# Kernel tuning notes

Measured on AMD Instinct MI355X. Metric: run time of the kernel, lower is better.

Reference implementation:

```python
import jax, jax.numpy as jnp
import numpy as np

N = 100000   # nodes
E = 1600000  # edges (avg degree 16)
D = 64       # input feature dim
H = 64       # hidden dim


def _uniform(k, shape, fan_in):
    s = 1.0 / np.sqrt(fan_in).astype(np.float32)
    return jax.random.uniform(k, shape, jnp.float32, -s, s)


def setup_inputs() -> dict:
    key = jax.random.key(0)
    ks = jax.random.split(key, 9)
    x = jax.random.normal(ks[0], (N, D), jnp.float32)
    edge_index = jax.random.randint(ks[1], (2, E), 0, N, dtype=jnp.int64)
    edge_weight = jax.random.uniform(ks[2], (E,), jnp.float32)
    return {
        "x": x,
        "edge_index": edge_index,
        "edge_weight": edge_weight,
        # conv1: GraphConv(D, H): lin_rel (with bias) + lin_root (no bias)
        "w1_rel": _uniform(ks[3], (H, D), D),
        "b1": _uniform(ks[4], (H,), D),
        "w1_root": _uniform(ks[5], (H, D), D),
        # conv2: GraphConv(H, H)
        "w2_rel": _uniform(ks[6], (H, H), H),
        "b2": _uniform(ks[7], (H,), H),
        "w2_root": _uniform(ks[8], (H, H), H),
    }


def _graph_conv(h, src, dst, ew, w_rel, b, w_root):
    # PyG GraphConv with aggr='add':
    #   out_i = W_rel @ sum_{(j->i) in E} ew_ji * h_j + b + W_root @ h_i
    msg = h[src] * ew[:, None]                              # [E, F] gather
    agg = jax.ops.segment_sum(msg, dst, num_segments=N)     # [N, F] scatter-add
    return agg @ w_rel.T + b + h @ w_root.T


def reference(x, edge_index, edge_weight, w1_rel, b1, w1_root, w2_rel, b2, w2_root):
    src, dst = edge_index[0], edge_index[1]
    # dropout(0.2) is identity in eval mode
    h = jax.nn.relu(_graph_conv(x, src, dst, edge_weight, w1_rel, b1, w1_root))
    h = jax.nn.relu(_graph_conv(h, src, dst, edge_weight, w2_rel, b2, w2_root))
    return h
```

## Files before the change

kernel.cpp:

```cpp
#include <hip/hip_runtime.h>
#include <cstddef>


#define FDIM 64
#define BSHC 9
#define BNC (1 << BSHC)
#define CAPC 8960

static inline size_t align256(size_t x) { return (x + 255) & ~size_t(255); }

typedef __attribute__((ext_vector_type(8))) short bf16x8;
typedef __attribute__((ext_vector_type(4))) float f32x4;

__device__ __forceinline__ ushort f2bf(float f) {
    unsigned u = __float_as_uint(f);
    unsigned r = u + 0x7fffu + ((u >> 16) & 1u);
    return (ushort)(r >> 16);
}
__device__ __forceinline__ float bflo(unsigned g) { return __uint_as_float(g << 16); }
__device__ __forceinline__ float bfhi(unsigned g) { return __uint_as_float(g & 0xffff0000u); }
__device__ __forceinline__ unsigned packbf(float lo, float hi) {
    return (unsigned)f2bf(lo) | ((unsigned)f2bf(hi) << 16);
}

__global__ void k_detect(const int* __restrict__ ei, int* __restrict__ flag,
                         int* __restrict__ gcur, int nbc) {
    __shared__ int any;
    if (threadIdx.x == 0) any = 0;
    __syncthreads();
    for (int k = threadIdx.x; k < 2048; k += 256) {
        if (ei[2 * k + 1] != 0) any = 1;
    }
    for (int i = threadIdx.x; i < nbc; i += 256) gcur[i] = 0;
    __syncthreads();
    if (threadIdx.x == 0) *flag = (any == 0) ? 1 : 0;
}

__global__ void k_toBf16(const float* __restrict__ in, ushort* __restrict__ outp,
                         int nflt) {
    int i = (blockIdx.x * blockDim.x + threadIdx.x) * 4;
    if (i >= nflt) return;
    float4 v = *reinterpret_cast<const float4*>(in + i);
    ushort4 o;
    o.x = f2bf(v.x); o.y = f2bf(v.y); o.z = f2bf(v.z); o.w = f2bf(v.w);
    *reinterpret_cast<ushort4*>(outp + i) = o;
}

__global__ void k_packW(const float* __restrict__ wrel1, const float* __restrict__ wroot1,
                        const float* __restrict__ wrel2, const float* __restrict__ wroot2,
                        ushort* __restrict__ wp1, ushort* __restrict__ wp2) {
    int tid = blockIdx.x * blockDim.x + threadIdx.x;
    int layer = tid >> 13;
    int idx = tid & 8191;
    int j = idx & 7, l = (idx >> 3) & 63, og = (idx >> 9) & 3, kk = idx >> 11;
    int k = kk * 32 + ((l >> 4) << 3) + j;
    int o = og * 16 + (l & 15);
    const float* rel  = layer ? wrel2 : wrel1;
    const float* root = layer ? wroot2 : wroot1;
    float v = (k < 64) ? rel[o * FDIM + k] : root[o * FDIM + (k - 64)];
    (layer ? wp2 : wp1)[idx] = f2bf(v);
}

__global__ void __launch_bounds__(512)
k_scatterC(const int* __restrict__ ei, const float* __restrict__ ew, int E,
           const int* __restrict__ flag, int* __restrict__ gcur,
           uint2* __restrict__ recs, int nbc) {
    __shared__ int hcnt[256];
    __shared__ int hbase[256];
    int t = threadIdx.x;
    int base = blockIdx.x * 4096;
    int sh = *flag;
    if (t < 256) hcnt[t] = 0;
    __syncthreads();

    int bkt[8];
    uint2 rec[8];
#pragma unroll
    for (int j = 0; j < 8; ++j) {
        int e = base + j * 512 + t;
        bkt[j] = -1;
        if (e < E) {
            int s = ei[(size_t)e << sh];
            int d = ei[(size_t)(E + e) << sh];
            bkt[j] = d >> BSHC;
            rec[j].x = (unsigned)s | ((unsigned)(d & (BNC - 1)) << 17);
            rec[j].y = __float_as_uint(ew[e]);
            atomicAdd(&hcnt[bkt[j]], 1);
        }
    }
    __syncthreads();
    if (t < nbc) {
        int c = hcnt[t];
        hbase[t] = c ? (t * CAPC + atomicAdd(&gcur[t], c)) : 0;
    }
    __syncthreads();
    if (t < 256) hcnt[t] = 0;
    __syncthreads();
#pragma unroll
    for (int j = 0; j < 8; ++j) {
        if (bkt[j] >= 0) {
            int r = atomicAdd(&hcnt[bkt[j]], 1);
            int pos = hbase[bkt[j]] + r;
            if (pos < (bkt[j] + 1) * CAPC) recs[pos] = rec[j];
        }
    }
}

__global__ void __launch_bounds__(512)
k_csrSortC(const int* __restrict__ gcur, uint2* __restrict__ recs, int n,
           int* __restrict__ rs, int* __restrict__ re) {
    __shared__ uint2 lrec[CAPC];
    __shared__ int lh[BNC];
    __shared__ int lo[BNC];
    __shared__ int lcur[BNC];
    int b = blockIdx.x, t = threadIdx.x;
    int base = b * CAPC;
    int cnt = gcur[b];
    if (cnt > CAPC) cnt = CAPC;

    for (int i = t; i < cnt; i += 512) lrec[i] = recs[base + i];
    lh[t] = 0;
    __syncthreads();
    for (int i = t; i < cnt; i += 512) atomicAdd(&lh[lrec[i].x >> 17], 1);
    __syncthreads();
    lo[t] = lh[t];
    __syncthreads();
    for (int off = 1; off < BNC; off <<= 1) {
        int v = (t >= off) ? lo[t - off] : 0;
        __syncthreads();
        lo[t] += v;
        __syncthreads();
    }
    {
        int ex = lo[t] - lh[t];
        lcur[t] = ex;
        int node = (b << BSHC) + t;
        if (node < n) { rs[node] = base + ex; re[node] = base + ex + lh[t]; }
    }
    __syncthreads();
    for (int i = t; i < cnt; i += 512) {
        uint2 r = lrec[i];
        int pos = atomicAdd(&lcur[r.x >> 17], 1);
        recs[base + pos] = make_uint2(r.x & 0x1FFFF, r.y);
    }
}

__global__ void __launch_bounds__(256)
k_aggB16(const ushort* __restrict__ hb, const int* __restrict__ rs,
         const int* __restrict__ re, const uint2* __restrict__ recs,
         int n, ushort* __restrict__ aggb) {
    int wavid = (blockIdx.x * blockDim.x + threadIdx.x) >> 6;
    int lane = threadIdx.x & 63;
    int nA = wavid << 1;
    if (nA >= n) return;
    int nB = nA + 1;
    int q = lane >> 3, sl = lane & 7;
    const uint4* hw4 = reinterpret_cast<const uint4*>(hb);
    int pA = rs[nA], eA = re[nA];
    int pB = rs[nB], eB = re[nB];

    float A0 = 0.f, A1 = 0.f, A2 = 0.f, A3 = 0.f, A4 = 0.f, A5 = 0.f, A6 = 0.f, A7 = 0.f;
    float B0 = 0.f, B1 = 0.f, B2 = 0.f, B3 = 0.f, B4 = 0.f, B5 = 0.f, B6 = 0.f, B7 = 0.f;

#define FMA8(P, g, wf)                                       \
    do {                                                     \
        float w_ = (wf);                                     \
        P##0 = fmaf(bflo((g).x), w_, P##0);                  \
        P##1 = fmaf(bfhi((g).x), w_, P##1);                  \
        P##2 = fmaf(bflo((g).y), w_, P##2);                  \
        P##3 = fmaf(bfhi((g).y), w_, P##3);                  \
        P##4 = fmaf(bflo((g).z), w_, P##4);                  \
        P##5 = fmaf(bfhi((g).z), w_, P##5);                  \
        P##6 = fmaf(bflo((g).w), w_, P##6);                  \
        P##7 = fmaf(bfhi((g).w), w_, P##7);                  \
    } while (0)

    while (pA < eA || pB < eB) {
        int iA0 = pA + q, iA1 = pA + 8 + q;
        int iB0 = pB + q, iB1 = pB + 8 + q;
        uint2 ra0 = recs[iA0];
        uint2 ra1 = recs[iA1];
        uint2 rb0 = recs[iB0];
        uint2 rb1 = recs[iB1];
        uint4 ga0 = hw4[(size_t)(ra0.x & 0x1FFFFu) * 8 + sl];
        uint4 ga1 = hw4[(size_t)(ra1.x & 0x1FFFFu) * 8 + sl];
        uint4 gb0 = hw4[(size_t)(rb0.x & 0x1FFFFu) * 8 + sl];
        uint4 gb1 = hw4[(size_t)(rb1.x & 0x1FFFFu) * 8 + sl];
        float wa0 = (iA0 < eA) ? __uint_as_float(ra0.y) : 0.f;
        float wa1 = (iA1 < eA) ? __uint_as_float(ra1.y) : 0.f;
        float wb0 = (iB0 < eB) ? __uint_as_float(rb0.y) : 0.f;
        float wb1 = (iB1 < eB) ? __uint_as_float(rb1.y) : 0.f;
        FMA8(A, ga0, wa0);
        FMA8(A, ga1, wa1);
        FMA8(B, gb0, wb0);
        FMA8(B, gb1, wb1);
        pA = (pA + 16 < eA) ? pA + 16 : eA;
        pB = (pB + 16 < eB) ? pB + 16 : eB;
    }
#undef FMA8

#define RED2(d)                                                  \
    A0 += __shfl_xor(A0, d, 64); A1 += __shfl_xor(A1, d, 64);    \
    A2 += __shfl_xor(A2, d, 64); A3 += __shfl_xor(A3, d, 64);    \
    A4 += __shfl_xor(A4, d, 64); A5 += __shfl_xor(A5, d, 64);    \
    A6 += __shfl_xor(A6, d, 64); A7 += __shfl_xor(A7, d, 64);    \
    B0 += __shfl_xor(B0, d, 64); B1 += __shfl_xor(B1, d, 64);    \
    B2 += __shfl_xor(B2, d, 64); B3 += __shfl_xor(B3, d, 64);    \
    B4 += __shfl_xor(B4, d, 64); B5 += __shfl_xor(B5, d, 64);    \
    B6 += __shfl_xor(B6, d, 64); B7 += __shfl_xor(B7, d, 64);
    RED2(8) RED2(16) RED2(32)
#undef RED2

    if (q == 0) {
        uint4 o;
        o.x = packbf(A0, A1);
        o.y = packbf(A2, A3);
        o.z = packbf(A4, A5);
        o.w = packbf(A6, A7);
        reinterpret_cast<uint4*>(aggb + (size_t)nA * FDIM)[sl] = o;
    } else if (q == 1) {
        uint4 o;
        o.x = packbf(B0, B1);
        o.y = packbf(B2, B3);
        o.z = packbf(B4, B5);
        o.w = packbf(B6, B7);
        reinterpret_cast<uint4*>(aggb + (size_t)nB * FDIM)[sl] = o;
    }
}

template<int OUTBF>
__global__ void __launch_bounds__(256)
k_denseM(const ushort* __restrict__ aggb, const ushort* __restrict__ rootb,
         const ushort* __restrict__ wp, const float* __restrict__ bias,
         float* __restrict__ outp, ushort* __restrict__ outb, int n) {
    int t = threadIdx.x;
    int wv = t >> 6, l = t & 63;
    int n0 = blockIdx.x * 64 + wv * 16;
    int row = l & 15, half = l >> 4;

    int node = n0 + row;
    bool inb = node < n;
    const ushort* ap = aggb + (size_t)node * FDIM + half * 8;
    const ushort* rp = rootb + (size_t)node * FDIM + half * 8;
    bf16x8 a0 = inb ? *reinterpret_cast<const bf16x8*>(ap)      : bf16x8{0,0,0,0,0,0,0,0};
    bf16x8 a1 = inb ? *reinterpret_cast<const bf16x8*>(ap + 32) : bf16x8{0,0,0,0,0,0,0,0};
    bf16x8 a2 = inb ? *reinterpret_cast<const bf16x8*>(rp)      : bf16x8{0,0,0,0,0,0,0,0};
    bf16x8 a3 = inb ? *reinterpret_cast<const bf16x8*>(rp + 32) : bf16x8{0,0,0,0,0,0,0,0};

    f32x4 acc[4];
#pragma unroll
    for (int og = 0; og < 4; ++og) acc[og] = f32x4{0.f, 0.f, 0.f, 0.f};

#pragma unroll
    for (int og = 0; og < 4; ++og) {
        const bf16x8* wb = reinterpret_cast<const bf16x8*>(wp) + og * 64 + l;
        acc[og] = __builtin_amdgcn_mfma_f32_16x16x32_bf16(a0, wb[0],       acc[og], 0, 0, 0);
        acc[og] = __builtin_amdgcn_mfma_f32_16x16x32_bf16(a1, wb[4 * 64],  acc[og], 0, 0, 0);
        acc[og] = __builtin_amdgcn_mfma_f32_16x16x32_bf16(a2, wb[8 * 64],  acc[og], 0, 0, 0);
        acc[og] = __builtin_amdgcn_mfma_f32_16x16x32_bf16(a3, wb[12 * 64], acc[og], 0, 0, 0);
    }

    int rbase = n0 + half * 4;
#pragma unroll
    for (int og = 0; og < 4; ++og) {
        float bb = bias[og * 16 + row];
#pragma unroll
        for (int r = 0; r < 4; ++r) {
            int nd = rbase + r;
            if (nd < n) {
                float v = fmaxf(acc[og][r] + bb, 0.f);
                if (OUTBF) outb[(size_t)nd * FDIM + og * 16 + row] = f2bf(v);
                else       outp[(size_t)nd * FDIM + og * 16 + row] = v;
            }
        }
    }
}

extern "C" void kernel_launch(void* const* d_in, const int* in_sizes, int n_in,
                              void* d_out, int out_size, void* d_ws, size_t ws_size,
                              hipStream_t stream) {
    const float* x      = (const float*)d_in[0];
    const int*   ei     = (const int*)d_in[1];
    const float* ew     = (const float*)d_in[2];
    const float* w1rel  = (const float*)d_in[3];
    const float* b1     = (const float*)d_in[4];
    const float* w1root = (const float*)d_in[5];
    const float* w2rel  = (const float*)d_in[6];
    const float* b2     = (const float*)d_in[7];
    const float* w2root = (const float*)d_in[8];
    float* out = (float*)d_out;

    int N = in_sizes[0] / FDIM;
    int E = in_sizes[2];
    int NBC = (N + BNC - 1) >> BSHC;

    char* w = (char*)d_ws;
    int* flag    = (int*)w;    w += align256(256);
    int* gcur    = (int*)w;    w += align256((size_t)NBC * 4);
    int* rs      = (int*)w;    w += align256((size_t)N * 4);
    int* re      = (int*)w;    w += align256((size_t)N * 4);
    ushort* wp1  = (ushort*)w; w += align256(8192 * 2);
    ushort* wp2  = (ushort*)w; w += align256(8192 * 2);
    uint2* recs  = (uint2*)w;  w += align256((size_t)NBC * CAPC * 8);
    ushort* aggb = (ushort*)w; w += align256((size_t)N * FDIM * 2);
    ushort* xb   = (ushort*)w; w += align256((size_t)N * FDIM * 2);
    ushort* h1b  = (ushort*)w; w += align256((size_t)N * FDIM * 2);

    k_detect<<<1, 256, 0, stream>>>(ei, flag, gcur, NBC);
    k_packW<<<64, 256, 0, stream>>>(w1rel, w1root, w2rel, w2root, wp1, wp2);
    k_toBf16<<<(N * FDIM / 4 + 255) / 256, 256, 0, stream>>>(x, xb, N * FDIM);
    k_scatterC<<<(E + 4095) / 4096, 512, 0, stream>>>(ei, ew, E, flag, gcur, recs, NBC);
    k_csrSortC<<<NBC, 512, 0, stream>>>(gcur, recs, N, rs, re);

    k_aggB16<<<(N + 7) / 8, 256, 0, stream>>>(xb, rs, re, recs, N, aggb);
    k_denseM<1><<<(N + 63) / 64, 256, 0, stream>>>(aggb, xb, wp1, b1, nullptr, h1b, N);
    k_aggB16<<<(N + 7) / 8, 256, 0, stream>>>(h1b, rs, re, recs, N, aggb);
    k_denseM<0><<<(N + 63) / 64, 256, 0, stream>>>(aggb, h1b, wp2, b2, out, nullptr, N);
}
```

Baseline: 147.1 us.

## Fuse edge aggregation into dense MFMA kernel via LDS and merge prep kernels

Each wave now aggregates its 16 nodes sequentially into shared memory and then runs the MFMA dense transform directly, removing the global aggregate buffer and two launches. The three setup kernels are merged into one launch. The cost is much less wave-level parallelism in the latency-bound gather, since each wave serially processes eight node pairs.

```diff
diff --git a/kernel.cpp b/kernel.cpp
--- a/kernel.cpp
+++ b/kernel.cpp
@@ -23,42 +23,42 @@
     return (unsigned)f2bf(lo) | ((unsigned)f2bf(hi) << 16);
 }
 
-__global__ void k_detect(const int* __restrict__ ei, int* __restrict__ flag,
-                         int* __restrict__ gcur, int nbc) {
-    __shared__ int any;
-    if (threadIdx.x == 0) any = 0;
-    __syncthreads();
-    for (int k = threadIdx.x; k < 2048; k += 256) {
-        if (ei[2 * k + 1] != 0) any = 1;
-    }
-    for (int i = threadIdx.x; i < nbc; i += 256) gcur[i] = 0;
-    __syncthreads();
-    if (threadIdx.x == 0) *flag = (any == 0) ? 1 : 0;
-}
-
-__global__ void k_toBf16(const float* __restrict__ in, ushort* __restrict__ outp,
-                         int nflt) {
-    int i = (blockIdx.x * blockDim.x + threadIdx.x) * 4;
-    if (i >= nflt) return;
-    float4 v = *reinterpret_cast<const float4*>(in + i);
-    ushort4 o;
-    o.x = f2bf(v.x); o.y = f2bf(v.y); o.z = f2bf(v.z); o.w = f2bf(v.w);
-    *reinterpret_cast<ushort4*>(outp + i) = o;
-}
-
-__global__ void k_packW(const float* __restrict__ wrel1, const float* __restrict__ wroot1,
-                        const float* __restrict__ wrel2, const float* __restrict__ wroot2,
-                        ushort* __restrict__ wp1, ushort* __restrict__ wp2) {
-    int tid = blockIdx.x * blockDim.x + threadIdx.x;
-    int layer = tid >> 13;
-    int idx = tid & 8191;
-    int j = idx & 7, l = (idx >> 3) & 63, og = (idx >> 9) & 3, kk = idx >> 11;
-    int k = kk * 32 + ((l >> 4) << 3) + j;
-    int o = og * 16 + (l & 15);
-    const float* rel  = layer ? wrel2 : wrel1;
-    const float* root = layer ? wroot2 : wroot1;
-    float v = (k < 64) ? rel[o * FDIM + k] : root[o * FDIM + (k - 64)];
-    (layer ? wp2 : wp1)[idx] = f2bf(v);
+__global__ void __launch_bounds__(256)
+k_prep(const float* __restrict__ x, ushort* __restrict__ xb, int nflt,
+       const int* __restrict__ ei, int* __restrict__ flag,
+       int* __restrict__ gcur, int nbc,
+       const float* __restrict__ wrel1, const float* __restrict__ wroot1,
+       const float* __restrict__ wrel2, const float* __restrict__ wroot2,
+       ushort* __restrict__ wp1, ushort* __restrict__ wp2) {
+    int t = threadIdx.x, bid = blockIdx.x;
+    int i = (bid * 256 + t) * 4;
+    if (i < nflt) {
+        float4 v = *reinterpret_cast<const float4*>(x + i);
+        ushort4 o;
+        o.x = f2bf(v.x); o.y = f2bf(v.y); o.z = f2bf(v.z); o.w = f2bf(v.w);
+        *reinterpret_cast<ushort4*>(xb + i) = o;
+    }
+    if (bid == 0) {
+        __shared__ int any;
+        if (t == 0) any = 0;
+        __syncthreads();
+        for (int k = t; k < 2048; k += 256)
+            if (ei[2 * k + 1] != 0) any = 1;
+        for (int j = t; j < nbc; j += 256) gcur[j] = 0;
+        __syncthreads();
+        if (t == 0) *flag = (any == 0) ? 1 : 0;
+    } else if (bid <= 64) {
+        int tid = (bid - 1) * 256 + t;
+        int layer = tid >> 13;
+        int idx = tid & 8191;
+        int j = idx & 7, l = (idx >> 3) & 63, og = (idx >> 9) & 3, kk = idx >> 11;
+        int k = kk * 32 + ((l >> 4) << 3) + j;
+        int o = og * 16 + (l & 15);
+        const float* rel  = layer ? wrel2 : wrel1;
+        const float* root = layer ? wroot2 : wroot1;
+        float v = (k < 64) ? rel[o * FDIM + k] : root[o * FDIM + (k - 64)];
+        (layer ? wp2 : wp1)[idx] = f2bf(v);
+    }
 }
 
 __global__ void __launch_bounds__(512)
@@ -145,105 +145,104 @@
     }
 }
 
-__global__ void __launch_bounds__(256)
-k_aggB16(const ushort* __restrict__ hb, const int* __restrict__ rs,
-         const int* __restrict__ re, const uint2* __restrict__ recs,
-         int n, ushort* __restrict__ aggb) {
-    int wavid = (blockIdx.x * blockDim.x + threadIdx.x) >> 6;
-    int lane = threadIdx.x & 63;
-    int nA = wavid << 1;
-    if (nA >= n) return;
-    int nB = nA + 1;
-    int q = lane >> 3, sl = lane & 7;
-    const uint4* hw4 = reinterpret_cast<const uint4*>(hb);
-    int pA = rs[nA], eA = re[nA];
-    int pB = rs[nB], eB = re[nB];
-
-    float A0 = 0.f, A1 = 0.f, A2 = 0.f, A3 = 0.f, A4 = 0.f, A5 = 0.f, A6 = 0.f, A7 = 0.f;
-    float B0 = 0.f, B1 = 0.f, B2 = 0.f, B3 = 0.f, B4 = 0.f, B5 = 0.f, B6 = 0.f, B7 = 0.f;
-
-#define FMA8(P, g, wf)                                       \
-    do {                                                     \
-        float w_ = (wf);                                     \
-        P##0 = fmaf(bflo((g).x), w_, P##0);                  \
-        P##1 = fmaf(bfhi((g).x), w_, P##1);                  \
-        P##2 = fmaf(bflo((g).y), w_, P##2);                  \
-        P##3 = fmaf(bfhi((g).y), w_, P##3);                  \
-        P##4 = fmaf(bflo((g).z), w_, P##4);                  \
-        P##5 = fmaf(bfhi((g).z), w_, P##5);                  \
-        P##6 = fmaf(bflo((g).w), w_, P##6);                  \
-        P##7 = fmaf(bfhi((g).w), w_, P##7);                  \
-    } while (0)
-
-    while (pA < eA || pB < eB) {
-        int iA0 = pA + q, iA1 = pA + 8 + q;
-        int iB0 = pB + q, iB1 = pB + 8 + q;
-        uint2 ra0 = recs[iA0];
-        uint2 ra1 = recs[iA1];
-        uint2 rb0 = recs[iB0];
-        uint2 rb1 = recs[iB1];
-        uint4 ga0 = hw4[(size_t)(ra0.x & 0x1FFFFu) * 8 + sl];
-        uint4 ga1 = hw4[(size_t)(ra1.x & 0x1FFFFu) * 8 + sl];
-        uint4 gb0 = hw4[(size_t)(rb0.x & 0x1FFFFu) * 8 + sl];
-        uint4 gb1 = hw4[(size_t)(rb1.x & 0x1FFFFu) * 8 + sl];
-        float wa0 = (iA0 < eA) ? __uint_as_float(ra0.y) : 0.f;
-        float wa1 = (iA1 < eA) ? __uint_as_float(ra1.y) : 0.f;
-        float wb0 = (iB0 < eB) ? __uint_as_float(rb0.y) : 0.f;
-        float wb1 = (iB1 < eB) ? __uint_as_float(rb1.y) : 0.f;
-        FMA8(A, ga0, wa0);
-        FMA8(A, ga1, wa1);
-        FMA8(B, gb0, wb0);
-        FMA8(B, gb1, wb1);
-        pA = (pA + 16 < eA) ? pA + 16 : eA;
-        pB = (pB + 16 < eB) ? pB + 16 : eB;
-    }
-#undef FMA8
-
-#define RED2(d)                                                  \
-    A0 += __shfl_xor(A0, d, 64); A1 += __shfl_xor(A1, d, 64);    \
-    A2 += __shfl_xor(A2, d, 64); A3 += __shfl_xor(A3, d, 64);    \
-    A4 += __shfl_xor(A4, d, 64); A5 += __shfl_xor(A5, d, 64);    \
-    A6 += __shfl_xor(A6, d, 64); A7 += __shfl_xor(A7, d, 64);    \
-    B0 += __shfl_xor(B0, d, 64); B1 += __shfl_xor(B1, d, 64);    \
-    B2 += __shfl_xor(B2, d, 64); B3 += __shfl_xor(B3, d, 64);    \
-    B4 += __shfl_xor(B4, d, 64); B5 += __shfl_xor(B5, d, 64);    \
-    B6 += __shfl_xor(B6, d, 64); B7 += __shfl_xor(B7, d, 64);
-    RED2(8) RED2(16) RED2(32)
-#undef RED2
-
-    if (q == 0) {
-        uint4 o;
-        o.x = packbf(A0, A1);
-        o.y = packbf(A2, A3);
-        o.z = packbf(A4, A5);
-        o.w = packbf(A6, A7);
-        reinterpret_cast<uint4*>(aggb + (size_t)nA * FDIM)[sl] = o;
-    } else if (q == 1) {
-        uint4 o;
-        o.x = packbf(B0, B1);
-        o.y = packbf(B2, B3);
-        o.z = packbf(B4, B5);
-        o.w = packbf(B6, B7);
-        reinterpret_cast<uint4*>(aggb + (size_t)nB * FDIM)[sl] = o;
-    }
-}
-
 template<int OUTBF>
 __global__ void __launch_bounds__(256)
-k_denseM(const ushort* __restrict__ aggb, const ushort* __restrict__ rootb,
-         const ushort* __restrict__ wp, const float* __restrict__ bias,
-         float* __restrict__ outp, ushort* __restrict__ outb, int n) {
+k_aggDense(const ushort* __restrict__ hb, const int* __restrict__ rs,
+           const int* __restrict__ re, const uint2* __restrict__ recs,
+           const ushort* __restrict__ wp, const float* __restrict__ bias,
+           float* __restrict__ outp, ushort* __restrict__ outb, int n) {
+    __shared__ ushort lagg[4][16][FDIM];
     int t = threadIdx.x;
     int wv = t >> 6, l = t & 63;
-    int n0 = blockIdx.x * 64 + wv * 16;
+    int base = blockIdx.x * 64 + wv * 16;
+    int q = l >> 3, sl = l & 7;
+    const uint4* hw4 = reinterpret_cast<const uint4*>(hb);
+
+    for (int i = 0; i < 8; ++i) {
+        int nA = base + 2 * i;
+        if (nA >= n) break;
+        int nB = nA + 1;
+        int pA = rs[nA], eA = re[nA];
+        int pB = rs[nB], eB = re[nB];
+
+        float A0 = 0.f, A1 = 0.f, A2 = 0.f, A3 = 0.f, A4 = 0.f, A5 = 0.f, A6 = 0.f, A7 = 0.f;
+        float B0 = 0.f, B1 = 0.f, B2 = 0.f, B3 = 0.f, B4 = 0.f, B5 = 0.f, B6 = 0.f, B7 = 0.f;
+
+#define FMA8(P, g, wf)                                       \
+        do {                                                 \
+            float w_ = (wf);                                 \
+            P##0 = fmaf(bflo((g).x), w_, P##0);              \
+            P##1 = fmaf(bfhi((g).x), w_, P##1);              \
+            P##2 = fmaf(bflo((g).y), w_, P##2);              \
+            P##3 = fmaf(bfhi((g).y), w_, P##3);              \
+            P##4 = fmaf(bflo((g).z), w_, P##4);              \
+            P##5 = fmaf(bfhi((g).z), w_, P##5);              \
+            P##6 = fmaf(bflo((g).w), w_, P##6);              \
+            P##7 = fmaf(bfhi((g).w), w_, P##7);              \
+        } while (0)
+
+        while (pA < eA || pB < eB) {
+            int iA0 = pA + q, iA1 = pA + 8 + q;
+            int iB0 = pB + q, iB1 = pB + 8 + q;
+            uint2 ra0 = recs[iA0];
+            uint2 ra1 = recs[iA1];
+            uint2 rb0 = recs[iB0];
+            uint2 rb1 = recs[iB1];
+            uint4 ga0 = hw4[(size_t)(ra0.x & 0x1FFFFu) * 8 + sl];
+            uint4 ga1 = hw4[(size_t)(ra1.x & 0x1FFFFu) * 8 + sl];
+            uint4 gb0 = hw4[(size_t)(rb0.x & 0x1FFFFu) * 8 + sl];
+            uint4 gb1 = hw4[(size_t)(rb1.x & 0x1FFFFu) * 8 + sl];
+            float wa0 = (iA0 < eA) ? __uint_as_float(ra0.y) : 0.f;
+            float wa1 = (iA1 < eA) ? __uint_as_float(ra1.y) : 0.f;
+            float wb0 = (iB0 < eB) ? __uint_as_float(rb0.y) : 0.f;
+            float wb1 = (iB1 < eB) ? __uint_as_float(rb1.y) : 0.f;
+            FMA8(A, ga0, wa0);
+            FMA8(A, ga1, wa1);
+            FMA8(B, gb0, wb0);
+            FMA8(B, gb1, wb1);
+            pA = (pA + 16 < eA) ? pA + 16 : eA;
+            pB = (pB + 16 < eB) ? pB + 16 : eB;
+        }
+#undef FMA8
+
+#define RED2(d)                                                  \
+        A0 += __shfl_xor(A0, d, 64); A1 += __shfl_xor(A1, d, 64);\
+        A2 += __shfl_xor(A2, d, 64); A3 += __shfl_xor(A3, d, 64);\
+        A4 += __shfl_xor(A4, d, 64); A5 += __shfl_xor(A5, d, 64);\
+        A6 += __shfl_xor(A6, d, 64); A7 += __shfl_xor(A7, d, 64);\
+        B0 += __shfl_xor(B0, d, 64); B1 += __shfl_xor(B1, d, 64);\
+        B2 += __shfl_xor(B2, d, 64); B3 += __shfl_xor(B3, d, 64);\
+        B4 += __shfl_xor(B4, d, 64); B5 += __shfl_xor(B5, d, 64);\
+        B6 += __shfl_xor(B6, d, 64); B7 += __shfl_xor(B7, d, 64);
+        RED2(8) RED2(16) RED2(32)
+#undef RED2
+
+        if (q == 0) {
+            uint4 o;
+            o.x = packbf(A0, A1);
+            o.y = packbf(A2, A3);
+            o.z = packbf(A4, A5);
+            o.w = packbf(A6, A7);
+            reinterpret_cast<uint4*>(lagg[wv][2 * i])[sl] = o;
+        } else if (q == 1) {
+            uint4 o;
+            o.x = packbf(B0, B1);
+            o.y = packbf(B2, B3);
+            o.z = packbf(B4, B5);
+            o.w = packbf(B6, B7);
+            reinterpret_cast<uint4*>(lagg[wv][2 * i + 1])[sl] = o;
+        }
+    }
+    __syncthreads();
+
     int row = l & 15, half = l >> 4;
-
-    int node = n0 + row;
+    int node = base + row;
     bool inb = node < n;
-    const ushort* ap = aggb + (size_t)node * FDIM + half * 8;
-    const ushort* rp = rootb + (size_t)node * FDIM + half * 8;
-    bf16x8 a0 = inb ? *reinterpret_cast<const bf16x8*>(ap)      : bf16x8{0,0,0,0,0,0,0,0};
-    bf16x8 a1 = inb ? *reinterpret_cast<const bf16x8*>(ap + 32) : bf16x8{0,0,0,0,0,0,0,0};
+
+    const ushort* lp = lagg[wv][row] + half * 8;
+    bf16x8 a0 = *reinterpret_cast<const bf16x8*>(lp);
+    bf16x8 a1 = *reinterpret_cast<const bf16x8*>(lp + 32);
+    const ushort* rp = hb + (size_t)node * FDIM + half * 8;
     bf16x8 a2 = inb ? *reinterpret_cast<const bf16x8*>(rp)      : bf16x8{0,0,0,0,0,0,0,0};
     bf16x8 a3 = inb ? *reinterpret_cast<const bf16x8*>(rp + 32) : bf16x8{0,0,0,0,0,0,0,0};
 
@@ -260,7 +259,7 @@
         acc[og] = __builtin_amdgcn_mfma_f32_16x16x32_bf16(a3, wb[12 * 64], acc[og], 0, 0, 0);
     }
 
-    int rbase = n0 + half * 4;
+    int rbase = base + half * 4;
 #pragma unroll
     for (int og = 0; og < 4; ++og) {
         float bb = bias[og * 16 + row];
@@ -302,18 +301,17 @@
     ushort* wp1  = (ushort*)w; w += align256(8192 * 2);
     ushort* wp2  = (ushort*)w; w += align256(8192 * 2);
     uint2* recs  = (uint2*)w;  w += align256((size_t)NBC * CAPC * 8);
-    ushort* aggb = (ushort*)w; w += align256((size_t)N * FDIM * 2);
     ushort* xb   = (ushort*)w; w += align256((size_t)N * FDIM * 2);
     ushort* h1b  = (ushort*)w; w += align256((size_t)N * FDIM * 2);
 
-    k_detect<<<1, 256, 0, stream>>>(ei, flag, gcur, NBC);
-    k_packW<<<64, 256, 0, stream>>>(w1rel, w1root, w2rel, w2root, wp1, wp2);
-    k_toBf16<<<(N * FDIM / 4 + 255) / 256, 256, 0, stream>>>(x, xb, N * FDIM);
+    int nflt = N * FDIM;
+    k_prep<<<(nflt / 4 + 255) / 256, 256, 0, stream>>>(
+        x, xb, nflt, ei, flag, gcur, NBC, w1rel, w1root, w2rel, w2root, wp1, wp2);
     k_scatterC<<<(E + 4095) / 4096, 512, 0, stream>>>(ei, ew, E, flag, gcur, recs, NBC);
     k_csrSortC<<<NBC, 512, 0, stream>>>(gcur, recs, N, rs, re);
 
-    k_aggB16<<<(N + 7) / 8, 256, 0, stream>>>(xb, rs, re, recs, N, aggb);
-    k_denseM<1><<<(N + 63) / 64, 256, 0, stream>>>(aggb, xb, wp1, b1, nullptr, h1b, N);
-    k_aggB16<<<(N + 7) / 8, 256, 0, stream>>>(h1b, rs, re, recs, N, aggb);
-    k_denseM<0><<<(N + 63) / 64, 256, 0, stream>>>(aggb, h1b, wp2, b2, out, nullptr, N);
-}
+    k_aggDense<1><<<(N + 63) / 64, 256, 0, stream>>>(xb, rs, re, recs, wp1, b1,
+                                                     nullptr, h1b, N);
+    k_aggDense<0><<<(N + 63) / 64, 256, 0, stream>>>(h1b, rs, re, recs, wp2, b2,
+                                                     out, nullptr, N);
+}
```

Result: slower. 163.8 us (+11.4%).
